# Kernel tuning notes

Hardware: AMD Instinct MI355X
Metric: run time of the kernel (lower is better)

The kernel has to match this reference:

```python
import jax, jax.numpy as jnp
import numpy as np

B, N, D_IN, D_OUT = 2, 4096, 768, 768


def setup_inputs() -> dict:
    key = jax.random.key(0)
    kx, kq, kk, kv = jax.random.split(key, 4)
    x = jax.random.normal(kx, (B, N, D_IN), dtype=jnp.float32)
    # Linear(d_in, d_out, bias=False) weights, stored as [d_in, d_out]
    scale = 1.0 / np.sqrt(D_IN)
    Wq = jax.random.normal(kq, (D_IN, D_OUT), dtype=jnp.float32) * scale
    Wk = jax.random.normal(kk, (D_IN, D_OUT), dtype=jnp.float32) * scale
    Wv = jax.random.normal(kv, (D_IN, D_OUT), dtype=jnp.float32) * scale
    return {"x": x, "Wq": Wq, "Wk": Wk, "Wv": Wv}


def reference(x, Wq, Wk, Wv):
    # q,k,v: [B, N, D_OUT]
    q = jnp.einsum('bnd,de->bne', x, Wq)
    k = jnp.einsum('bnd,de->bne', x, Wk)
    v = jnp.einsum('bnd,de->bne', x, Wv)
    # Full [B, N, N] score matrix (naive attention, as in source).
    # NOTE: source's masked_fill is non-in-place and discarded, so NO causal
    # mask is actually applied -- reproduced faithfully here.
    scores = jnp.einsum('bqe,bke->bqk', q, k) / jnp.sqrt(jnp.float32(k.shape[-1]))
    weights = jax.nn.softmax(scores, axis=-1)
    # dropout rate 0.0 / eval mode -> identity
    out = jnp.einsum('bqk,bke->bqe', weights, v)  # [B, N, D_OUT]
    return out
```

## Files before the change

kernel.cpp:

```cpp
#include <hip/hip_runtime.h>

typedef __bf16 bf16x8 __attribute__((ext_vector_type(8)));
typedef float f32x4 __attribute__((ext_vector_type(4)));
typedef unsigned short us8 __attribute__((ext_vector_type(8)));

#define GAS __attribute__((address_space(1)))
#define LAS __attribute__((address_space(3)))

__device__ __forceinline__ unsigned short f32_to_bf16(float f) {
    unsigned int u = __float_as_uint(f);
    u += 0x7FFFu + ((u >> 16) & 1u);
    return (unsigned short)(u >> 16);
}

__device__ __forceinline__ float bf16_to_f32(unsigned short h) {
    return __uint_as_float((unsigned int)h << 16);
}

__device__ __forceinline__ void load16(const unsigned short* g, unsigned short* l) {
    __builtin_amdgcn_global_load_lds((GAS unsigned int*)g, (LAS unsigned int*)l, 16, 0, 0);
}

__global__ __launch_bounds__(256) void convert_f32_bf16(
    const float* __restrict__ in, unsigned short* __restrict__ out, int n4)
{
    int i = blockIdx.x * 256 + threadIdx.x;
    if (i < n4) {
        float4 v = ((const float4*)in)[i];
        ushort4 o;
        o.x = f32_to_bf16(v.x); o.y = f32_to_bf16(v.y);
        o.z = f32_to_bf16(v.z); o.w = f32_to_bf16(v.w);
        ((ushort4*)out)[i] = o;
    }
}

__global__ __launch_bounds__(1024) void transpose_w(
    const float* __restrict__ W0, const float* __restrict__ W1, const float* __restrict__ W2,
    unsigned short* __restrict__ T0, unsigned short* __restrict__ T1, unsigned short* __restrict__ T2)
{
    __shared__ float tile[32][33];
    const float* W = (blockIdx.z == 0) ? W0 : (blockIdx.z == 1) ? W1 : W2;
    unsigned short* T = (blockIdx.z == 0) ? T0 : (blockIdx.z == 1) ? T1 : T2;
    int r0 = blockIdx.y * 32, c0 = blockIdx.x * 32;
    tile[threadIdx.y][threadIdx.x] = W[(size_t)(r0 + threadIdx.y) * 768 + c0 + threadIdx.x];
    __syncthreads();
    T[(size_t)(c0 + threadIdx.y) * 768 + r0 + threadIdx.x] = f32_to_bf16(tile[threadIdx.x][threadIdx.y]);
}

__global__ __launch_bounds__(1024) void transpose_v(
    const unsigned short* __restrict__ V, unsigned short* __restrict__ Vt)
{
    __shared__ unsigned short tile[32][33];
    int r0 = blockIdx.y * 32, c0 = blockIdx.x * 32;
    tile[threadIdx.y][threadIdx.x] = V[(size_t)(r0 + threadIdx.y) * 768 + c0 + threadIdx.x];
    __syncthreads();
    Vt[(size_t)(c0 + threadIdx.y) * 8192 + r0 + threadIdx.x] = tile[threadIdx.x][threadIdx.y];
}

template <typename CT>
__global__ __launch_bounds__(256) void gemm_nt(
    const unsigned short* __restrict__ A, const unsigned short* __restrict__ B,
    CT* __restrict__ C, int K, int lda, int ldb, int ldc,
    size_t sA, size_t sB, size_t sC, float alpha)
{
    A += (size_t)blockIdx.z * sA;
    B += (size_t)blockIdx.z * sB;
    C += (size_t)blockIdx.z * sC;
    const int m0 = blockIdx.y * 128;
    const int n0 = blockIdx.x * 128;
    const int t = threadIdx.x;
    const int lane = t & 63;
    const int w = t >> 6;
    const int wm = (w >> 1) * 64;
    const int wn = (w & 1) * 64;

    __shared__ unsigned short At[128 * 64];
    __shared__ unsigned short Bt[128 * 64];

    f32x4 acc[4][4];
#pragma unroll
    for (int i = 0; i < 4; ++i)
#pragma unroll
        for (int j = 0; j < 4; ++j) acc[i][j] = (f32x4){0.f, 0.f, 0.f, 0.f};

    const int r15 = lane & 15;
    const int qa = lane >> 4;

    for (int k0 = 0; k0 < K; k0 += 64) {
#pragma unroll
        for (int i = 0; i < 4; ++i) {
            const int c = i * 256 + t;
            const int row = c >> 3;
            const int cc = (c & 7) ^ (row & 7);
            load16(A + (size_t)(m0 + row) * lda + k0 + cc * 8, &At[c * 8]);
            load16(B + (size_t)(n0 + row) * ldb + k0 + cc * 8, &Bt[c * 8]);
        }
        __syncthreads();

#pragma unroll
        for (int ks = 0; ks < 2; ++ks) {
            bf16x8 af[4], bf[4];
#pragma unroll
            for (int mi = 0; mi < 4; ++mi) {
                const int row = wm + mi * 16 + r15;
                af[mi] = *(const bf16x8*)&At[row * 64 + (((ks << 2) + qa) ^ (row & 7)) * 8];
            }
#pragma unroll
            for (int ni = 0; ni < 4; ++ni) {
                const int row = wn + ni * 16 + r15;
                bf[ni] = *(const bf16x8*)&Bt[row * 64 + (((ks << 2) + qa) ^ (row & 7)) * 8];
            }
#pragma unroll
            for (int mi = 0; mi < 4; ++mi)
#pragma unroll
                for (int ni = 0; ni < 4; ++ni)
                    acc[mi][ni] = __builtin_amdgcn_mfma_f32_16x16x32_bf16(
                        af[mi], bf[ni], acc[mi][ni], 0, 0, 0);
        }
        __syncthreads();
    }

    const int cr = (lane >> 4) * 4;
#pragma unroll
    for (int mi = 0; mi < 4; ++mi) {
#pragma unroll
        for (int ni = 0; ni < 4; ++ni) {
            const int gm = m0 + wm + mi * 16 + cr;
            const int gn = n0 + wn + ni * 16 + r15;
#pragma unroll
            for (int r = 0; r < 4; ++r) {
                float v = alpha * acc[mi][ni][r];
                if constexpr (sizeof(CT) == 2)
                    C[(size_t)(gm + r) * ldc + gn] = (CT)f32_to_bf16(v);
                else
                    C[(size_t)(gm + r) * ldc + gn] = v;
            }
        }
    }
}

__global__ __launch_bounds__(256) void gemm_s_exp(
    const unsigned short* __restrict__ Q, const unsigned short* __restrict__ Kb,
    unsigned short* __restrict__ Sexp, float alpha)
{
    const unsigned short* A = Q + (size_t)blockIdx.z * 3145728;
    const unsigned short* B = Kb + (size_t)blockIdx.z * 3145728;
    unsigned short* C = Sexp + (size_t)blockIdx.z * 16777216;
    const int lda = 768, ldb = 768, ldc = 4096;
    const int m0 = blockIdx.y * 128;
    const int n0 = blockIdx.x * 128;
    const int t = threadIdx.x;
    const int lane = t & 63;
    const int w = t >> 6;
    const int wm = (w >> 1) * 64;
    const int wn = (w & 1) * 64;

    __shared__ unsigned short At[128 * 64];
    __shared__ unsigned short Bt[128 * 64];

    f32x4 acc[4][4];
#pragma unroll
    for (int i = 0; i < 4; ++i)
#pragma unroll
        for (int j = 0; j < 4; ++j) acc[i][j] = (f32x4){0.f, 0.f, 0.f, 0.f};

    const int r15 = lane & 15;
    const int qa = lane >> 4;

    for (int k0 = 0; k0 < 768; k0 += 64) {
#pragma unroll
        for (int i = 0; i < 4; ++i) {
            const int c = i * 256 + t;
            const int row = c >> 3;
            const int cc = (c & 7) ^ (row & 7);
            load16(A + (size_t)(m0 + row) * lda + k0 + cc * 8, &At[c * 8]);
            load16(B + (size_t)(n0 + row) * ldb + k0 + cc * 8, &Bt[c * 8]);
        }
        __syncthreads();

#pragma unroll
        for (int ks = 0; ks < 2; ++ks) {
            bf16x8 af[4], bf[4];
#pragma unroll
            for (int mi = 0; mi < 4; ++mi) {
                const int row = wm + mi * 16 + r15;
                af[mi] = *(const bf16x8*)&At[row * 64 + (((ks << 2) + qa) ^ (row & 7)) * 8];
            }
#pragma unroll
            for (int ni = 0; ni < 4; ++ni) {
                const int row = wn + ni * 16 + r15;
                bf[ni] = *(const bf16x8*)&Bt[row * 64 + (((ks << 2) + qa) ^ (row & 7)) * 8];
            }
#pragma unroll
            for (int mi = 0; mi < 4; ++mi)
#pragma unroll
                for (int ni = 0; ni < 4; ++ni)
                    acc[mi][ni] = __builtin_amdgcn_mfma_f32_16x16x32_bf16(
                        af[mi], bf[ni], acc[mi][ni], 0, 0, 0);
        }
        __syncthreads();
    }

    const int cr = (lane >> 4) * 4;
#pragma unroll
    for (int mi = 0; mi < 4; ++mi)
#pragma unroll
        for (int ni = 0; ni < 4; ++ni) {
            const int gm = m0 + wm + mi * 16 + cr;
            const int gn = n0 + wn + ni * 16 + r15;
#pragma unroll
            for (int r = 0; r < 4; ++r)
                C[(size_t)(gm + r) * ldc + gn] = f32_to_bf16(__expf(alpha * acc[mi][ni][r]));
        }
}

__global__ __launch_bounds__(256) void lsum_rows(
    const unsigned short* __restrict__ Sexp, float* __restrict__ lsum)
{
    const size_t row = blockIdx.x;
    const unsigned short* s = Sexp + row * 4096;
    const int t = threadIdx.x;
    const int wv = t >> 6, ln = t & 63;

    us8 a = ((const us8*)s)[t];
    us8 b = ((const us8*)s)[t + 256];
    float lsumv = 0.f;
#pragma unroll
    for (int j = 0; j < 8; ++j) lsumv += bf16_to_f32(a[j]) + bf16_to_f32(b[j]);
#pragma unroll
    for (int off = 32; off > 0; off >>= 1) lsumv += __shfl_down(lsumv, off, 64);
    __shared__ float red[4];
    if (ln == 0) red[wv] = lsumv;
    __syncthreads();
    if (t == 0) lsum[row] = red[0] + red[1] + red[2] + red[3];
}

__global__ __launch_bounds__(256) void gemm_nt_splitk(
    const unsigned short* __restrict__ P, const unsigned short* __restrict__ Vt,
    float* __restrict__ Part)
{
    const int f = blockIdx.x;
    const int r8 = f & 7;
    const int tq = f >> 3;
    const int n  = tq % 6;
    const int v  = tq / 6;
    const int u  = v * 8 + r8;
    const int batch = u & 1;
    const int split = (u >> 1) & 3;
    const int m = u >> 3;

    const unsigned short* A = P + (size_t)batch * 16777216 + (size_t)split * 1024;
    const unsigned short* B = Vt + (size_t)batch * 4096 + (size_t)split * 1024;
    float* C = Part + (size_t)(split * 2 + batch) * 3145728;
    const int lda = 4096, ldb = 8192, ldc = 768;
    const int m0 = m * 128;
    const int n0 = n * 128;
    const int t = threadIdx.x;
    const int lane = t & 63;
    const int w = t >> 6;
    const int wm = (w >> 1) * 64;
    const int wn = (w & 1) * 64;

    __shared__ unsigned short At[128 * 64];
    __shared__ unsigned short Bt[128 * 64];

    f32x4 acc[4][4];
#pragma unroll
    for (int i = 0; i < 4; ++i)
#pragma unroll
        for (int j = 0; j < 4; ++j) acc[i][j] = (f32x4){0.f, 0.f, 0.f, 0.f};

    const int r15 = lane & 15;
    const int qa = lane >> 4;

    for (int k0 = 0; k0 < 1024; k0 += 64) {
#pragma unroll
        for (int i = 0; i < 4; ++i) {
            const int c = i * 256 + t;
            const int row = c >> 3;
            const int cc = (c & 7) ^ (row & 7);
            load16(A + (size_t)(m0 + row) * lda + k0 + cc * 8, &At[c * 8]);
            load16(B + (size_t)(n0 + row) * ldb + k0 + cc * 8, &Bt[c * 8]);
        }
        __syncthreads();

#pragma unroll
        for (int ks = 0; ks < 2; ++ks) {
            bf16x8 af[4], bf[4];
#pragma unroll
            for (int mi = 0; mi < 4; ++mi) {
                const int row = wm + mi * 16 + r15;
                af[mi] = *(const bf16x8*)&At[row * 64 + (((ks << 2) + qa) ^ (row & 7)) * 8];
            }
#pragma unroll
            for (int ni = 0; ni < 4; ++ni) {
                const int row = wn + ni * 16 + r15;
                bf[ni] = *(const bf16x8*)&Bt[row * 64 + (((ks << 2) + qa) ^ (row & 7)) * 8];
            }
#pragma unroll
            for (int mi = 0; mi < 4; ++mi)
#pragma unroll
                for (int ni = 0; ni < 4; ++ni)
                    acc[mi][ni] = __builtin_amdgcn_mfma_f32_16x16x32_bf16(
                        af[mi], bf[ni], acc[mi][ni], 0, 0, 0);
        }
        __syncthreads();
    }

    const int cr = (lane >> 4) * 4;
#pragma unroll
    for (int mi = 0; mi < 4; ++mi) {
#pragma unroll
        for (int ni = 0; ni < 4; ++ni) {
            const int gm = m0 + wm + mi * 16 + cr;
            const int gn = n0 + wn + ni * 16 + r15;
#pragma unroll
            for (int r = 0; r < 4; ++r)
                C[(size_t)(gm + r) * ldc + gn] = acc[mi][ni][r];
        }
    }
}

__global__ __launch_bounds__(256) void reduce4_norm(
    const float* __restrict__ Part, const float* __restrict__ lsum,
    float* __restrict__ out)
{
    const size_t i = (size_t)blockIdx.x * 256 + threadIdx.x;
    const f32x4* p = (const f32x4*)Part;
    const float inv = 1.f / lsum[i / 192];
    f32x4 v = p[i] + p[i + 1572864] + p[i + 2 * 1572864] + p[i + 3 * 1572864];
    ((f32x4*)out)[i] = v * inv;
}

extern "C" void kernel_launch(void* const* d_in, const int* in_sizes, int n_in,
                              void* d_out, int out_size, void* d_ws, size_t ws_size,
                              hipStream_t stream) {
    const float* x  = (const float*)d_in[0];
    const float* Wq = (const float*)d_in[1];
    const float* Wk = (const float*)d_in[2];
    const float* Wv = (const float*)d_in[3];
    float* out = (float*)d_out;

    char* base = (char*)d_ws;
    size_t off = 0;
    auto alloc = [&](size_t b) { char* p = base + off; off += (b + 255) & ~(size_t)255; return p; };

    unsigned short* Xbf = (unsigned short*)alloc(8192ull * 768 * 2);
    unsigned short* WqT = (unsigned short*)alloc(768ull * 768 * 2);
    unsigned short* WkT = (unsigned short*)alloc(768ull * 768 * 2);
    unsigned short* WvT = (unsigned short*)alloc(768ull * 768 * 2);
    unsigned short* Qb  = (unsigned short*)alloc(8192ull * 768 * 2);
    unsigned short* Kb  = (unsigned short*)alloc(8192ull * 768 * 2);
    unsigned short* Vb  = (unsigned short*)alloc(8192ull * 768 * 2);
    unsigned short* Vt  = (unsigned short*)alloc(768ull * 8192 * 2);
    unsigned short* Sexp = (unsigned short*)alloc(2ull * 4096 * 4096 * 2);
    float*          Part = (float*)alloc(8ull * 3145728 * 4);
    float*          lsum = (float*)alloc(8192ull * 4);
    (void)ws_size; (void)in_sizes; (void)n_in; (void)out_size; (void)WkT;

    convert_f32_bf16<<<dim3(6144), dim3(256), 0, stream>>>(x, Xbf, 8192 * 768 / 4);
    transpose_w<<<dim3(24, 24, 3), dim3(32, 32), 0, stream>>>(Wq, Wk, Wv, WqT, WkT, WvT);
    gemm_nt<unsigned short><<<dim3(6, 64, 3), dim3(256), 0, stream>>>(
        Xbf, WqT, Qb, 768, 768, 768, 768,
         0,  589824,  6291456, 1.0f);
    transpose_v<<<dim3(24, 256), dim3(32, 32), 0, stream>>>(Vb, Vt);
    gemm_s_exp<<<dim3(32, 32, 2), dim3(256), 0, stream>>>(
        Qb, Kb, Sexp, 0.03608439182435161f);
    lsum_rows<<<dim3(8192), dim3(256), 0, stream>>>(Sexp, lsum);
    gemm_nt_splitk<<<dim3(1536), dim3(256), 0, stream>>>(Sexp, Vt, Part);
    reduce4_norm<<<dim3(6144), dim3(256), 0, stream>>>(Part, lsum, out);
}
```

Before: 304.3 us.

## Fuse row-sum into split-K reduction and store partials in bf16

```diff
diff --git a/kernel.cpp b/kernel.cpp
--- a/kernel.cpp
+++ b/kernel.cpp
@@ -214,30 +214,9 @@
         }
 }
 
-__global__ __launch_bounds__(256) void lsum_rows(
-    const unsigned short* __restrict__ Sexp, float* __restrict__ lsum)
-{
-    const size_t row = blockIdx.x;
-    const unsigned short* s = Sexp + row * 4096;
-    const int t = threadIdx.x;
-    const int wv = t >> 6, ln = t & 63;
-
-    us8 a = ((const us8*)s)[t];
-    us8 b = ((const us8*)s)[t + 256];
-    float lsumv = 0.f;
-#pragma unroll
-    for (int j = 0; j < 8; ++j) lsumv += bf16_to_f32(a[j]) + bf16_to_f32(b[j]);
-#pragma unroll
-    for (int off = 32; off > 0; off >>= 1) lsumv += __shfl_down(lsumv, off, 64);
-    __shared__ float red[4];
-    if (ln == 0) red[wv] = lsumv;
-    __syncthreads();
-    if (t == 0) lsum[row] = red[0] + red[1] + red[2] + red[3];
-}
-
 __global__ __launch_bounds__(256) void gemm_nt_splitk(
     const unsigned short* __restrict__ P, const unsigned short* __restrict__ Vt,
-    float* __restrict__ Part)
+    unsigned short* __restrict__ Part)
 {
     const int f = blockIdx.x;
     const int r8 = f & 7;
@@ -251,7 +230,7 @@
 
     const unsigned short* A = P + (size_t)batch * 16777216 + (size_t)split * 1024;
     const unsigned short* B = Vt + (size_t)batch * 4096 + (size_t)split * 1024;
-    float* C = Part + (size_t)(split * 2 + batch) * 3145728;
+    unsigned short* C = Part + (size_t)(split * 2 + batch) * 3145728;
     const int lda = 4096, ldb = 8192, ldc = 768;
     const int m0 = m * 128;
     const int n0 = n * 128;
@@ -316,20 +295,51 @@
             const int gn = n0 + wn + ni * 16 + r15;
 #pragma unroll
             for (int r = 0; r < 4; ++r)
-                C[(size_t)(gm + r) * ldc + gn] = acc[mi][ni][r];
-        }
-    }
-}
-
-__global__ __launch_bounds__(256) void reduce4_norm(
-    const float* __restrict__ Part, const float* __restrict__ lsum,
+                C[(size_t)(gm + r) * ldc + gn] = f32_to_bf16(acc[mi][ni][r]);
+        }
+    }
+}
+
+__global__ __launch_bounds__(256) void reduce_norm_rows(
+    const unsigned short* __restrict__ Sexp, const unsigned short* __restrict__ Part,
     float* __restrict__ out)
 {
-    const size_t i = (size_t)blockIdx.x * 256 + threadIdx.x;
-    const f32x4* p = (const f32x4*)Part;
-    const float inv = 1.f / lsum[i / 192];
-    f32x4 v = p[i] + p[i + 1572864] + p[i + 2 * 1572864] + p[i + 3 * 1572864];
-    ((f32x4*)out)[i] = v * inv;
+    const int g = blockIdx.x;
+    const int batch = g >> 12;
+    const int r = g & 4095;
+    const int t = threadIdx.x;
+    const int wv = t >> 6, ln = t & 63;
+
+    const unsigned short* srow = Sexp + (size_t)batch * 16777216 + (size_t)r * 4096;
+    us8 a = ((const us8*)srow)[t];
+    us8 b = ((const us8*)srow)[t + 256];
+    float s = 0.f;
+#pragma unroll
+    for (int j = 0; j < 8; ++j) s += bf16_to_f32(a[j]) + bf16_to_f32(b[j]);
+#pragma unroll
+    for (int off = 32; off > 0; off >>= 1) s += __shfl_down(s, off, 64);
+    __shared__ float red[4];
+    if (ln == 0) red[wv] = s;
+    __syncthreads();
+    const float inv = 1.f / (red[0] + red[1] + red[2] + red[3]);
+
+    if (t < 192) {
+        const int c = t * 4;
+        float4 acc = {0.f, 0.f, 0.f, 0.f};
+#pragma unroll
+        for (int sgroup = 0; sgroup < 4; ++sgroup) {
+            const unsigned short* p = Part
+                + ((size_t)(sgroup * 2 + batch) * 4096 + r) * 768 + c;
+            ushort4 u = *(const ushort4*)p;
+            acc.x += bf16_to_f32(u.x);
+            acc.y += bf16_to_f32(u.y);
+            acc.z += bf16_to_f32(u.z);
+            acc.w += bf16_to_f32(u.w);
+        }
+        float4 o;
+        o.x = acc.x * inv; o.y = acc.y * inv; o.z = acc.z * inv; o.w = acc.w * inv;
+        *(float4*)(out + (size_t)g * 768 + c) = o;
+    }
 }
 
 extern "C" void kernel_launch(void* const* d_in, const int* in_sizes, int n_in,
@@ -354,8 +364,7 @@
     unsigned short* Vb  = (unsigned short*)alloc(8192ull * 768 * 2);
     unsigned short* Vt  = (unsigned short*)alloc(768ull * 8192 * 2);
     unsigned short* Sexp = (unsigned short*)alloc(2ull * 4096 * 4096 * 2);
-    float*          Part = (float*)alloc(8ull * 3145728 * 4);
-    float*          lsum = (float*)alloc(8192ull * 4);
+    unsigned short* Part = (unsigned short*)alloc(8ull * 3145728 * 2);
     (void)ws_size; (void)in_sizes; (void)n_in; (void)out_size; (void)WkT;
 
     convert_f32_bf16<<<dim3(6144), dim3(256), 0, stream>>>(x, Xbf, 8192 * 768 / 4);
@@ -366,7 +375,6 @@
     transpose_v<<<dim3(24, 256), dim3(32, 32), 0, stream>>>(Vb, Vt);
     gemm_s_exp<<<dim3(32, 32, 2), dim3(256), 0, stream>>>(
         Qb, Kb, Sexp, 0.03608439182435161f);
-    lsum_rows<<<dim3(8192), dim3(256), 0, stream>>>(Sexp, lsum);
     gemm_nt_splitk<<<dim3(1536), dim3(256), 0, stream>>>(Sexp, Vt, Part);
-    reduce4_norm<<<dim3(6144), dim3(256), 0, stream>>>(Part, lsum, out);
-}
+    reduce_norm_rows<<<dim3(8192), dim3(256), 0, stream>>>(Sexp, Part, out);
+}
```

New measurement: 282.4 us. 7.2% less time.
